# Kernel optimization log

Hardware: AMD Instinct MI355X
Metric: run time of the kernel (lower is better)

Reference implementation:

```python
import jax, jax.numpy as jnp
import numpy as np

M, K, N, R = 8192, 4096, 4096, 64  # tokens, in_features, out_features, pod_rank


def _unpack_int4(packed):
    """Unpack bytes (stored as int32 in [0,256)) into signed int4 values in [-8,7].
    Low nibble is element 2k, high nibble is element 2k+1."""
    b = packed.astype(jnp.int32)
    low = ((b & 0xF) ^ 8) - 8
    high = (((b >> 4) & 0xF) ^ 8) - 8
    out = jnp.stack([low, high], axis=-1)
    return out.reshape(packed.shape[:-1] + (packed.shape[-1] * 2,))


def setup_inputs() -> dict:
    key = jax.random.key(0)
    ks = jax.random.split(key, 7)
    x_quant = jax.random.randint(ks[0], (M, K // 2), 0, 256, dtype=jnp.int32)
    x_scale = jax.random.uniform(ks[1], (M,), dtype=jnp.float32) * 0.01 + 1e-4
    weight = jax.random.randint(ks[2], (N, K // 2), 0, 256, dtype=jnp.int32)
    weight_scales = jax.random.uniform(ks[3], (N, 1), dtype=jnp.float32) * 0.01 + 1e-4
    bias = jax.random.normal(ks[4], (N,), dtype=jnp.float32) * 0.02
    x_r = jax.random.normal(ks[5], (M, R), dtype=jnp.float32)
    w_outlier = jax.random.normal(ks[6], (N, R), dtype=jnp.float32) * 0.02
    return {"x_quant": x_quant, "x_scale": x_scale, "weight": weight,
            "weight_scales": weight_scales, "bias": bias, "x_r": x_r,
            "w_outlier": w_outlier}


def reference(x_quant, x_scale, weight, weight_scales, bias, x_r, w_outlier):
    xi = _unpack_int4(x_quant)          # [M, K] int32 in [-8,7]
    wi = _unpack_int4(weight)           # [N, K] int32 in [-8,7]
    y_int = jnp.matmul(xi, wi.T)        # [M, N] int32 accumulator
    # dequant: per-token activation scale * per-channel weight scale, plus bias
    y = (y_int.astype(jnp.float32) * x_scale[:, None] * weight_scales.reshape(1, -1)
         + bias[None, :])
    # fused low-rank outlier correction: addmm_(x_r, w_outlier.T)
    y = y + jnp.matmul(x_r, w_outlier.T)
    return y
```

## Files before the change

### kernel.cpp

```cpp
#include <hip/hip_runtime.h>
#include <hip/hip_fp16.h>

typedef int      v4i __attribute__((ext_vector_type(4)));
typedef int      v2i __attribute__((ext_vector_type(2)));
typedef float    v4f __attribute__((ext_vector_type(4)));
typedef _Float16 v8h __attribute__((ext_vector_type(8)));
typedef _Float16 v4h __attribute__((ext_vector_type(4)));

#define MDIM 8192
#define NDIM 4096
#define KDIM 4096
#define RDIM 64
#define KW   (KDIM / 2)
#define BM 128
#define BN 128
#define BK 128

typedef const __attribute__((address_space(1))) int* gas_ptr;
typedef __attribute__((address_space(3))) int*       las_ptr;

__device__ __forceinline__ void unpack_w(v4i w, int& lo8, int& hi8) {
    unsigned p01 = __builtin_amdgcn_perm((unsigned)w.y, (unsigned)w.x, 0x0C0C0400u);
    unsigned p23 = __builtin_amdgcn_perm((unsigned)w.w, (unsigned)w.z, 0x0C0C0400u);
    unsigned b4  = __builtin_amdgcn_perm(p23, p01, 0x05040100u);
    unsigned lo = b4 & 0x0F0F0F0Fu;
    unsigned hi = (b4 >> 4) & 0x0F0F0F0Fu;
    lo8 = (int)(((lo ^ 0x08080808u) + 0x78787878u) ^ 0x80808080u);
    hi8 = (int)(((hi ^ 0x08080808u) + 0x78787878u) ^ 0x80808080u);
}

__global__ __launch_bounds__(256)
void repack_int4(const int* __restrict__ xq, const int* __restrict__ wq,
                 char* __restrict__ x8, char* __restrict__ w8)
{
    const size_t XCH = (size_t)MDIM * KW / 4;
    const size_t TCH = XCH + (size_t)NDIM * KW / 4;
    size_t stride = (size_t)gridDim.x * blockDim.x;
    for (size_t i = (size_t)blockIdx.x * blockDim.x + threadIdx.x; i < TCH; i += stride) {
        const int* src;
        char* dst;
        if (i < XCH) { src = xq + i * 4;        dst = x8 + i * 8; }
        else { size_t j = i - XCH; src = wq + j * 4; dst = w8 + j * 8; }
        v4i w = *(const v4i*)src;
        int lo8, hi8;
        unpack_w(w, lo8, hi8);
        *(v2i*)dst = (v2i){lo8, hi8};
    }
}

__global__ __launch_bounds__(256, 3)
void w4a4_gemm(const char* __restrict__ x8, const char* __restrict__ w8,
               const float* __restrict__ xsc, const float* __restrict__ wsc,
               const float* __restrict__ bias, const float* __restrict__ xr,
               const float* __restrict__ wo, float* __restrict__ out)
{
    __shared__ __align__(16) char As[128 * 144];
    __shared__ __align__(16) char Bs[128 * 144];
    __shared__ float xs_s[BM];
    __shared__ float ws_s[BN];
    __shared__ float bs_s[BN];

    const int tid  = threadIdx.x;
    const int lane = tid & 63;
    const int wid  = tid >> 6;
    const int wm   = wid >> 1;
    const int wn   = wid & 1;

    const int swz = (blockIdx.x & 7) * 256 + (blockIdx.x >> 3);
    const int bx  = swz & 31;
    const int by  = swz >> 5;

    if (tid < BM) {
        xs_s[tid] = xsc[by * BM + tid];
    } else {
        int n = tid - BM;
        ws_s[n] = wsc[bx * BN + n];
        bs_s[n] = bias[bx * BN + n];
    }

    const int srow8 = lane >> 3;
    const int scol  = (lane & 7) * 16;
    const char* gA = x8 + (size_t)(by * BM + srow8) * KDIM + scol;
    const char* gB = w8 + (size_t)(bx * BN + srow8) * KDIM + scol;

    v4i acc[4][4];
#pragma unroll
    for (int i = 0; i < 4; ++i)
#pragma unroll
        for (int j = 0; j < 4; ++j) acc[i][j] = (v4i){0, 0, 0, 0};

    const int lr  = lane & 15;
    const int lkb = (lane >> 4) * 16;

    for (int kt = 0; kt < KDIM / BK; ++kt) {
        const size_t kb = (size_t)kt * BK;
#pragma unroll
        for (int q = 0; q < 4; ++q) {
            const int chunk = wid * 4 + q;
            __builtin_amdgcn_global_load_lds(
                (gas_ptr)(const void*)(gA + (size_t)chunk * 8 * KDIM + kb),
                (las_ptr)(void*)(As + chunk * 1024), 16, 0, 0);
            __builtin_amdgcn_global_load_lds(
                (gas_ptr)(const void*)(gB + (size_t)chunk * 8 * KDIM + kb),
                (las_ptr)(void*)(Bs + chunk * 1024), 16, 0, 0);
        }
        __syncthreads();

#pragma unroll
        for (int ks = 0; ks < 2; ++ks) {
            v4i av[4], bv[4];
#pragma unroll
            for (int i = 0; i < 4; ++i)
                av[i] = *(const v4i*)(As + (wm * 64 + i * 16 + lr) * 128 + ks * 64 + lkb);
#pragma unroll
            for (int j = 0; j < 4; ++j)
                bv[j] = *(const v4i*)(Bs + (wn * 64 + j * 16 + lr) * 128 + ks * 64 + lkb);
#pragma unroll
            for (int i = 0; i < 4; ++i)
#pragma unroll
                for (int j = 0; j < 4; ++j)
                    acc[i][j] = __builtin_amdgcn_mfma_i32_16x16x64_i8(av[i], bv[j], acc[i][j], 0, 0, 0);
        }
        __syncthreads();
    }

    v4f facc[4][4];
#pragma unroll
    for (int i = 0; i < 4; ++i) {
        const int row0 = wm * 64 + i * 16 + (lane >> 4) * 4;
#pragma unroll
        for (int j = 0; j < 4; ++j) {
            const int col = wn * 64 + j * 16 + lr;
            const float sw = ws_s[col];
            const float bz = bs_s[col];
#pragma unroll
            for (int r = 0; r < 4; ++r)
                facc[i][j][r] = (float)acc[i][j][r] * xs_s[row0 + r] * sw + bz;
        }
    }

    _Float16* Xh = (_Float16*)As;
    _Float16* Wh = (_Float16*)Bs;
    const int srow   = tid >> 4;
    const int schunk = tid & 15;
#pragma unroll
    for (int p = 0; p < 8; ++p) {
        const int row = p * 16 + srow;
        float4 vx = *(const float4*)(xr + (size_t)(by * BM + row) * RDIM + schunk * 4);
        *(v4h*)(Xh + row * 72 + schunk * 4) =
            (v4h){(_Float16)vx.x, (_Float16)vx.y, (_Float16)vx.z, (_Float16)vx.w};
        float4 vw = *(const float4*)(wo + (size_t)(bx * BN + row) * RDIM + schunk * 4);
        *(v4h*)(Wh + row * 72 + schunk * 4) =
            (v4h){(_Float16)vw.x, (_Float16)vw.y, (_Float16)vw.z, (_Float16)vw.w};
    }
    __syncthreads();

    const int lkh = (lane >> 4) * 8;
#pragma unroll
    for (int ks = 0; ks < 2; ++ks) {
        v8h ah[4], bh[4];
#pragma unroll
        for (int i = 0; i < 4; ++i)
            ah[i] = *(const v8h*)(Xh + (wm * 64 + i * 16 + lr) * 72 + ks * 32 + lkh);
#pragma unroll
        for (int j = 0; j < 4; ++j)
            bh[j] = *(const v8h*)(Wh + (wn * 64 + j * 16 + lr) * 72 + ks * 32 + lkh);
#pragma unroll
        for (int i = 0; i < 4; ++i)
#pragma unroll
            for (int j = 0; j < 4; ++j)
                facc[i][j] = __builtin_amdgcn_mfma_f32_16x16x32_f16(ah[i], bh[j], facc[i][j], 0, 0, 0);
    }

#pragma unroll
    for (int i = 0; i < 4; ++i) {
        const int row0 = wm * 64 + i * 16 + (lane >> 4) * 4;
#pragma unroll
        for (int j = 0; j < 4; ++j) {
            const int col = wn * 64 + j * 16 + lr;
#pragma unroll
            for (int r = 0; r < 4; ++r)
                out[(size_t)(by * BM + row0 + r) * NDIM + (bx * BN + col)] = facc[i][j][r];
        }
    }
}

__global__ __launch_bounds__(256, 2)
void w4a4_fused(const int* __restrict__ xq, const float* __restrict__ xsc,
                const int* __restrict__ wq, const float* __restrict__ wsc,
                const float* __restrict__ bias, const float* __restrict__ xr,
                const float* __restrict__ wo, float* __restrict__ out)
{
    __shared__ __align__(16) char As[BM * 144];
    __shared__ __align__(16) char Bs[BN * 144];
    __shared__ float xs_s[BM];
    __shared__ float ws_s[BN];
    __shared__ float bs_s[BN];

    const int tid  = threadIdx.x;
    const int lane = tid & 63;
    const int wid  = tid >> 6;
    const int wm   = wid >> 1;
    const int wn   = wid & 1;
    const int bx   = blockIdx.x % (NDIM / BN);
    const int by   = blockIdx.x / (NDIM / BN);

    const int srow   = tid >> 4;
    const int schunk = tid & 15;

    if (tid < BM) {
        xs_s[tid] = xsc[by * BM + tid];
    } else {
        int n = tid - 128;
        ws_s[n] = wsc[bx * BN + n];
        bs_s[n] = bias[bx * BN + n];
    }

    const int* gA = xq + (size_t)(by * BM + srow) * KW + schunk * 4;
    const int* gB = wq + (size_t)(bx * BN + srow) * KW + schunk * 4;
    char* lA = As + srow * 144 + schunk * 8;
    char* lB = Bs + srow * 144 + schunk * 8;

    v4i acc[4][4];
#pragma unroll
    for (int i = 0; i < 4; ++i)
#pragma unroll
        for (int j = 0; j < 4; ++j) acc[i][j] = (v4i){0, 0, 0, 0};

    const int lr = lane & 15;
    const int lkb = (lane >> 4) * 16;

    for (int kt = 0; kt < KDIM / BK; ++kt) {
#pragma unroll
        for (int p = 0; p < 8; ++p) {
            v4i w = *(const v4i*)(gA + (size_t)p * 16 * KW + kt * (BK / 2));
            int lo8, hi8;
            unpack_w(w, lo8, hi8);
            *(v2i*)(lA + p * 16 * 144) = (v2i){lo8, hi8};
        }
#pragma unroll
        for (int p = 0; p < 8; ++p) {
            v4i w = *(const v4i*)(gB + (size_t)p * 16 * KW + kt * (BK / 2));
            int lo8, hi8;
            unpack_w(w, lo8, hi8);
            *(v2i*)(lB + p * 16 * 144) = (v2i){lo8, hi8};
        }
        __syncthreads();

#pragma unroll
        for (int ks = 0; ks < 2; ++ks) {
            v4i av[4], bv[4];
#pragma unroll
            for (int i = 0; i < 4; ++i)
                av[i] = *(const v4i*)(As + (wm * 64 + i * 16 + lr) * 144 + ks * 64 + lkb);
#pragma unroll
            for (int j = 0; j < 4; ++j)
                bv[j] = *(const v4i*)(Bs + (wn * 64 + j * 16 + lr) * 144 + ks * 64 + lkb);
#pragma unroll
            for (int i = 0; i < 4; ++i)
#pragma unroll
                for (int j = 0; j < 4; ++j)
                    acc[i][j] = __builtin_amdgcn_mfma_i32_16x16x64_i8(av[i], bv[j], acc[i][j], 0, 0, 0);
        }
        __syncthreads();
    }

    _Float16* Xh = (_Float16*)As;
    _Float16* Wh = (_Float16*)Bs;
#pragma unroll
    for (int p = 0; p < 8; ++p) {
        int row = p * 16 + srow;
        float4 vx = *(const float4*)(xr + (size_t)(by * BM + row) * RDIM + schunk * 4);
        *(v4h*)(Xh + row * 72 + schunk * 4) =
            (v4h){(_Float16)vx.x, (_Float16)vx.y, (_Float16)vx.z, (_Float16)vx.w};
        float4 vw = *(const float4*)(wo + (size_t)(bx * BN + row) * RDIM + schunk * 4);
        *(v4h*)(Wh + row * 72 + schunk * 4) =
            (v4h){(_Float16)vw.x, (_Float16)vw.y, (_Float16)vw.z, (_Float16)vw.w};
    }
    __syncthreads();

    v4f facc[4][4];
#pragma unroll
    for (int i = 0; i < 4; ++i)
#pragma unroll
        for (int j = 0; j < 4; ++j) facc[i][j] = (v4f){0.f, 0.f, 0.f, 0.f};

    const int lkh = (lane >> 4) * 8;
#pragma unroll
    for (int ks = 0; ks < 2; ++ks) {
        v8h ah[4], bh[4];
#pragma unroll
        for (int i = 0; i < 4; ++i)
            ah[i] = *(const v8h*)(Xh + (wm * 64 + i * 16 + lr) * 72 + ks * 32 + lkh);
#pragma unroll
        for (int j = 0; j < 4; ++j)
            bh[j] = *(const v8h*)(Wh + (wn * 64 + j * 16 + lr) * 72 + ks * 32 + lkh);
#pragma unroll
        for (int i = 0; i < 4; ++i)
#pragma unroll
            for (int j = 0; j < 4; ++j)
                facc[i][j] = __builtin_amdgcn_mfma_f32_16x16x32_f16(ah[i], bh[j], facc[i][j], 0, 0, 0);
    }

#pragma unroll
    for (int i = 0; i < 4; ++i) {
        int row0 = wm * 64 + i * 16 + (lane >> 4) * 4;
#pragma unroll
        for (int j = 0; j < 4; ++j) {
            int col = wn * 64 + j * 16 + lr;
            float sw = ws_s[col];
            float bz = bs_s[col];
#pragma unroll
            for (int r = 0; r < 4; ++r) {
                int row = row0 + r;
                float v = (float)acc[i][j][r] * xs_s[row] * sw + bz + facc[i][j][r];
                out[(size_t)(by * BM + row) * NDIM + (bx * BN + col)] = v;
            }
        }
    }
}

extern "C" void kernel_launch(void* const* d_in, const int* in_sizes, int n_in,
                              void* d_out, int out_size, void* d_ws, size_t ws_size,
                              hipStream_t stream) {
    const int*   xq   = (const int*)d_in[0];
    const float* xsc  = (const float*)d_in[1];
    const int*   wq   = (const int*)d_in[2];
    const float* wsc  = (const float*)d_in[3];
    const float* bias = (const float*)d_in[4];
    const float* xr   = (const float*)d_in[5];
    const float* wo   = (const float*)d_in[6];
    float* out = (float*)d_out;

    const size_t X8 = (size_t)MDIM * KDIM;
    const size_t W8 = (size_t)NDIM * KDIM;

    if (ws_size >= X8 + W8) {
        char* x8 = (char*)d_ws;
        char* w8 = x8 + X8;
        repack_int4<<<2048, 256, 0, stream>>>(xq, wq, x8, w8);
        w4a4_gemm<<<(MDIM / BM) * (NDIM / BN), 256, 0, stream>>>(
            x8, w8, xsc, wsc, bias, xr, wo, out);
    } else {
        w4a4_fused<<<(MDIM / BM) * (NDIM / BN), 256, 0, stream>>>(
            xq, xsc, wq, wsc, bias, xr, wo, out);
    }
}
```

Measured before the change: 207.3 us.

## Rewrite int8 GEMM as 256x256 tile, 8-wave, multi-stage pipelined kernel with swizzled LDS

Replaces the 128x128, 4-wave GEMM with a 256x256 tile computed by 512 threads. Global-to-LDS loads are split into 64-byte K sub-stages across a double-buffered ring, and prefetches are issued inside each MFMA phase with explicit vmcnt waits, barriers and setprio. The LDS layout uses an XOR swizzle to avoid bank conflicts, and the fp32 epilogue reuses the accumulator registers to save register pressure. The aim is to hide load latency behind MFMA and cut per-tile global traffic, at the cost of more LDS use, larger register demand and fewer blocks in flight.

```diff
diff --git a/kernel.cpp b/kernel.cpp
--- a/kernel.cpp
+++ b/kernel.cpp
@@ -12,12 +12,10 @@
 #define KDIM 4096
 #define RDIM 64
 #define KW   (KDIM / 2)
-#define BM 128
-#define BN 128
-#define BK 128
-
-typedef const __attribute__((address_space(1))) int* gas_ptr;
-typedef __attribute__((address_space(3))) int*       las_ptr;
+#define NT   (KDIM / 128)
+
+typedef const __attribute__((address_space(1))) char* gas_ptr;
+typedef __attribute__((address_space(3))) char*       las_ptr;
 
 __device__ __forceinline__ void unpack_w(v4i w, int& lo8, int& hi8) {
     unsigned p01 = __builtin_amdgcn_perm((unsigned)w.y, (unsigned)w.x, 0x0C0C0400u);
@@ -39,7 +37,7 @@
     for (size_t i = (size_t)blockIdx.x * blockDim.x + threadIdx.x; i < TCH; i += stride) {
         const int* src;
         char* dst;
-        if (i < XCH) { src = xq + i * 4;        dst = x8 + i * 8; }
+        if (i < XCH) { src = xq + i * 4; dst = x8 + i * 8; }
         else { size_t j = i - XCH; src = wq + j * 4; dst = w8 + j * 8; }
         v4i w = *(const v4i*)src;
         int lo8, hi8;
@@ -48,141 +46,185 @@
     }
 }
 
-__global__ __launch_bounds__(256, 3)
-void w4a4_gemm(const char* __restrict__ x8, const char* __restrict__ w8,
-               const float* __restrict__ xsc, const float* __restrict__ wsc,
-               const float* __restrict__ bias, const float* __restrict__ xr,
-               const float* __restrict__ wo, float* __restrict__ out)
+__device__ __forceinline__ void stage2(const char* g, char* l, int kt, int ks) {
+    const char* s = g + kt * 128 + ks * 64;
+    __builtin_amdgcn_global_load_lds((gas_ptr)(const void*)s,
+                                     (las_ptr)(void*)l, 16, 0, 0);
+    __builtin_amdgcn_global_load_lds((gas_ptr)(const void*)(s + (size_t)128 * KDIM),
+                                     (las_ptr)(void*)(l + 8192), 16, 0, 0);
+}
+
+#define VM4 asm volatile("s_waitcnt vmcnt(4)" ::: "memory")
+#define NOPW
+
+#define PHASE(PAR, MH, KS, STAGE_STMT, WAIT_STMT) do {                          \
+    const char* Ab = &Asub[PAR][KS][0];                                         \
+    const char* Bb = &Bsub[PAR][KS][0];                                         \
+    v4i a_[4], b_[4];                                                           \
+    _Pragma("unroll")                                                           \
+    for (int ii = 0; ii < 4; ++ii)                                              \
+        a_[ii] = *(const v4i*)(Ab + aoff + ((MH) * 4 + ii) * 1024);             \
+    _Pragma("unroll")                                                           \
+    for (int jj = 0; jj < 4; ++jj)                                              \
+        b_[jj] = *(const v4i*)(Bb + boff + jj * 1024);                          \
+    STAGE_STMT;                                                                 \
+    __builtin_amdgcn_s_barrier();                                               \
+    __builtin_amdgcn_s_setprio(1);                                              \
+    _Pragma("unroll")                                                           \
+    for (int ii = 0; ii < 4; ++ii)                                              \
+        _Pragma("unroll")                                                       \
+        for (int jj = 0; jj < 4; ++jj)                                          \
+            acc[(MH) * 4 + ii][jj] = __builtin_amdgcn_mfma_i32_16x16x64_i8(     \
+                a_[ii], b_[jj], acc[(MH) * 4 + ii][jj], 0, 0, 0);               \
+    __builtin_amdgcn_s_setprio(0);                                              \
+    WAIT_STMT;                                                                  \
+    asm volatile("s_barrier" ::: "memory");                                     \
+} while (0)
+
+__global__ __launch_bounds__(512, 2)
+void w4a4_gemm8(const char* __restrict__ x8, const char* __restrict__ w8,
+                const float* __restrict__ xsc, const float* __restrict__ wsc,
+                const float* __restrict__ bias, const float* __restrict__ xr,
+                const float* __restrict__ wo, float* __restrict__ out)
 {
-    __shared__ __align__(16) char As[128 * 144];
-    __shared__ __align__(16) char Bs[128 * 144];
-    __shared__ float xs_s[BM];
-    __shared__ float ws_s[BN];
-    __shared__ float bs_s[BN];
+    __shared__ __align__(16) char Asub[2][2][16384];
+    __shared__ __align__(16) char Bsub[2][2][16384];
+    __shared__ float xs_s[256];
+    __shared__ float ws_s[256];
+    __shared__ float bs_s[256];
 
     const int tid  = threadIdx.x;
     const int lane = tid & 63;
     const int wid  = tid >> 6;
-    const int wm   = wid >> 1;
-    const int wn   = wid & 1;
-
-    const int swz = (blockIdx.x & 7) * 256 + (blockIdx.x >> 3);
-    const int bx  = swz & 31;
-    const int by  = swz >> 5;
-
-    if (tid < BM) {
-        xs_s[tid] = xsc[by * BM + tid];
+    const int wm   = wid >> 2;
+    const int wn   = wid & 3;
+
+    const int s  = (blockIdx.x & 7) * 64 + (blockIdx.x >> 3);
+    const int by = s >> 4;
+    const int bx = s & 15;
+
+    if (tid < 256) {
+        xs_s[tid] = xsc[by * 256 + tid];
     } else {
-        int n = tid - BM;
-        ws_s[n] = wsc[bx * BN + n];
-        bs_s[n] = bias[bx * BN + n];
-    }
-
-    const int srow8 = lane >> 3;
-    const int scol  = (lane & 7) * 16;
-    const char* gA = x8 + (size_t)(by * BM + srow8) * KDIM + scol;
-    const char* gB = w8 + (size_t)(bx * BN + srow8) * KDIM + scol;
-
-    v4i acc[4][4];
-#pragma unroll
-    for (int i = 0; i < 4; ++i)
+        int n = tid - 256;
+        ws_s[n] = wsc[bx * 256 + n];
+        bs_s[n] = bias[bx * 256 + n];
+    }
+
+    const int srow = wid * 16 + (lane >> 2);
+    const int scol = ((lane & 3) * 16) ^ (((lane >> 3) & 3) << 4);
+    const char* gA = x8 + (size_t)(by * 256 + srow) * KDIM + scol;
+    const char* gB = w8 + (size_t)(bx * 256 + srow) * KDIM + scol;
+    const int ldsW = wid * 1024;
+
+    const int lr   = lane & 15;
+    const int cef  = ((lane >> 4) << 4) ^ (((lr >> 1) & 3) << 4);
+    const int aoff = (wm * 128 + lr) * 64 + cef;
+    const int boff = (wn * 64  + lr) * 64 + cef;
+
+    v4i acc[8][4];
+#pragma unroll
+    for (int i = 0; i < 8; ++i)
 #pragma unroll
         for (int j = 0; j < 4; ++j) acc[i][j] = (v4i){0, 0, 0, 0};
 
-    const int lr  = lane & 15;
-    const int lkb = (lane >> 4) * 16;
-
-    for (int kt = 0; kt < KDIM / BK; ++kt) {
-        const size_t kb = (size_t)kt * BK;
-#pragma unroll
-        for (int q = 0; q < 4; ++q) {
-            const int chunk = wid * 4 + q;
-            __builtin_amdgcn_global_load_lds(
-                (gas_ptr)(const void*)(gA + (size_t)chunk * 8 * KDIM + kb),
-                (las_ptr)(void*)(As + chunk * 1024), 16, 0, 0);
-            __builtin_amdgcn_global_load_lds(
-                (gas_ptr)(const void*)(gB + (size_t)chunk * 8 * KDIM + kb),
-                (las_ptr)(void*)(Bs + chunk * 1024), 16, 0, 0);
-        }
-        __syncthreads();
-
-#pragma unroll
-        for (int ks = 0; ks < 2; ++ks) {
-            v4i av[4], bv[4];
-#pragma unroll
-            for (int i = 0; i < 4; ++i)
-                av[i] = *(const v4i*)(As + (wm * 64 + i * 16 + lr) * 128 + ks * 64 + lkb);
-#pragma unroll
-            for (int j = 0; j < 4; ++j)
-                bv[j] = *(const v4i*)(Bs + (wn * 64 + j * 16 + lr) * 128 + ks * 64 + lkb);
-#pragma unroll
-            for (int i = 0; i < 4; ++i)
-#pragma unroll
-                for (int j = 0; j < 4; ++j)
-                    acc[i][j] = __builtin_amdgcn_mfma_i32_16x16x64_i8(av[i], bv[j], acc[i][j], 0, 0, 0);
-        }
-        __syncthreads();
-    }
-
-    v4f facc[4][4];
-#pragma unroll
-    for (int i = 0; i < 4; ++i) {
-        const int row0 = wm * 64 + i * 16 + (lane >> 4) * 4;
+    stage2(gA, &Asub[0][0][ldsW], 0, 0);
+    stage2(gB, &Bsub[0][0][ldsW], 0, 0);
+    stage2(gA, &Asub[0][1][ldsW], 0, 1);
+    stage2(gB, &Bsub[0][1][ldsW], 0, 1);
+    stage2(gA, &Asub[1][0][ldsW], 1, 0);
+    stage2(gB, &Bsub[1][0][ldsW], 1, 0);
+    asm volatile("s_waitcnt vmcnt(4)" ::: "memory");
+    asm volatile("s_barrier" ::: "memory");
+
+    for (int it = 0; it < NT / 2; ++it) {
+        const int kt1 = 2 * it + 1;
+        const int kt2 = (2 * it + 2 < NT) ? 2 * it + 2 : NT - 1;
+        const int kt3 = (2 * it + 3 < NT) ? 2 * it + 3 : NT - 1;
+        PHASE(0, 0, 0, stage2(gA, &Asub[1][1][ldsW], kt1, 1), NOPW);
+        PHASE(0, 1, 0, stage2(gB, &Bsub[1][1][ldsW], kt1, 1), NOPW);
+        PHASE(0, 0, 1, stage2(gA, &Asub[0][0][ldsW], kt2, 0), NOPW);
+        PHASE(0, 1, 1, stage2(gB, &Bsub[0][0][ldsW], kt2, 0), VM4);
+        PHASE(1, 0, 0, stage2(gA, &Asub[0][1][ldsW], kt2, 1), NOPW);
+        PHASE(1, 1, 0, stage2(gB, &Bsub[0][1][ldsW], kt2, 1), NOPW);
+        PHASE(1, 0, 1, stage2(gA, &Asub[1][0][ldsW], kt3, 0), NOPW);
+        PHASE(1, 1, 1, stage2(gB, &Bsub[1][0][ldsW], kt3, 0), VM4);
+    }
+
+    asm volatile("s_waitcnt vmcnt(0)" ::: "memory");
+    asm volatile("s_barrier" ::: "memory");
+
+    _Float16* Xh = (_Float16*)&Asub[0][0][0];
+    _Float16* Wh = (_Float16*)&Bsub[0][0][0];
+    {
+        const int rr = tid >> 3;
+        const int c8 = (tid & 7) * 8;
+#pragma unroll
+        for (int p = 0; p < 4; ++p) {
+            const int row = p * 64 + rr;
+            v4f x0 = *(const v4f*)(xr + (size_t)(by * 256 + row) * RDIM + c8);
+            v4f x1 = *(const v4f*)(xr + (size_t)(by * 256 + row) * RDIM + c8 + 4);
+            v8h hx = {(_Float16)x0[0], (_Float16)x0[1], (_Float16)x0[2], (_Float16)x0[3],
+                      (_Float16)x1[0], (_Float16)x1[1], (_Float16)x1[2], (_Float16)x1[3]};
+            *(v8h*)((char*)Xh + (size_t)row * 144 + c8 * 2) = hx;
+            v4f w0 = *(const v4f*)(wo + (size_t)(bx * 256 + row) * RDIM + c8);
+            v4f w1 = *(const v4f*)(wo + (size_t)(bx * 256 + row) * RDIM + c8 + 4);
+            v8h hw = {(_Float16)w0[0], (_Float16)w0[1], (_Float16)w0[2], (_Float16)w0[3],
+                      (_Float16)w1[0], (_Float16)w1[1], (_Float16)w1[2], (_Float16)w1[3]};
+            *(v8h*)((char*)Wh + (size_t)row * 144 + c8 * 2) = hw;
+        }
+    }
+
+#pragma unroll
+    for (int i = 0; i < 8; ++i) {
+        const int r0 = wm * 128 + i * 16 + ((lane >> 4) << 2);
+        const v4f xs4 = *(const v4f*)&xs_s[r0];
 #pragma unroll
         for (int j = 0; j < 4; ++j) {
             const int col = wn * 64 + j * 16 + lr;
             const float sw = ws_s[col];
             const float bz = bs_s[col];
+            v4f f;
 #pragma unroll
             for (int r = 0; r < 4; ++r)
-                facc[i][j][r] = (float)acc[i][j][r] * xs_s[row0 + r] * sw + bz;
-        }
-    }
-
-    _Float16* Xh = (_Float16*)As;
-    _Float16* Wh = (_Float16*)Bs;
-    const int srow   = tid >> 4;
-    const int schunk = tid & 15;
-#pragma unroll
-    for (int p = 0; p < 8; ++p) {
-        const int row = p * 16 + srow;
-        float4 vx = *(const float4*)(xr + (size_t)(by * BM + row) * RDIM + schunk * 4);
-        *(v4h*)(Xh + row * 72 + schunk * 4) =
-            (v4h){(_Float16)vx.x, (_Float16)vx.y, (_Float16)vx.z, (_Float16)vx.w};
-        float4 vw = *(const float4*)(wo + (size_t)(bx * BN + row) * RDIM + schunk * 4);
-        *(v4h*)(Wh + row * 72 + schunk * 4) =
-            (v4h){(_Float16)vw.x, (_Float16)vw.y, (_Float16)vw.z, (_Float16)vw.w};
+                f[r] = (float)acc[i][j][r] * xs4[r] * sw + bz;
+            acc[i][j] = __builtin_bit_cast(v4i, f);
+        }
     }
     __syncthreads();
 
-    const int lkh = (lane >> 4) * 8;
 #pragma unroll
     for (int ks = 0; ks < 2; ++ks) {
-        v8h ah[4], bh[4];
-#pragma unroll
-        for (int i = 0; i < 4; ++i)
-            ah[i] = *(const v8h*)(Xh + (wm * 64 + i * 16 + lr) * 72 + ks * 32 + lkh);
+        v8h ah[8], bh[4];
+#pragma unroll
+        for (int i = 0; i < 8; ++i)
+            ah[i] = *(const v8h*)((const char*)Xh +
+                     (size_t)(wm * 128 + i * 16 + lr) * 144 + ks * 64 + ((lane >> 4) << 4));
 #pragma unroll
         for (int j = 0; j < 4; ++j)
-            bh[j] = *(const v8h*)(Wh + (wn * 64 + j * 16 + lr) * 72 + ks * 32 + lkh);
-#pragma unroll
-        for (int i = 0; i < 4; ++i)
-#pragma unroll
-            for (int j = 0; j < 4; ++j)
-                facc[i][j] = __builtin_amdgcn_mfma_f32_16x16x32_f16(ah[i], bh[j], facc[i][j], 0, 0, 0);
-    }
-
-#pragma unroll
-    for (int i = 0; i < 4; ++i) {
-        const int row0 = wm * 64 + i * 16 + (lane >> 4) * 4;
+            bh[j] = *(const v8h*)((const char*)Wh +
+                     (size_t)(wn * 64 + j * 16 + lr) * 144 + ks * 64 + ((lane >> 4) << 4));
+#pragma unroll
+        for (int i = 0; i < 8; ++i)
+#pragma unroll
+            for (int j = 0; j < 4; ++j) {
+                v4f c = __builtin_bit_cast(v4f, acc[i][j]);
+                c = __builtin_amdgcn_mfma_f32_16x16x32_f16(ah[i], bh[j], c, 0, 0, 0);
+                acc[i][j] = __builtin_bit_cast(v4i, c);
+            }
+    }
+
+    const size_t obase = (size_t)(by * 256 + wm * 128 + ((lane >> 4) << 2)) * NDIM
+                       + bx * 256 + wn * 64 + lr;
+#pragma unroll
+    for (int i = 0; i < 8; ++i)
 #pragma unroll
         for (int j = 0; j < 4; ++j) {
-            const int col = wn * 64 + j * 16 + lr;
+            v4f f = __builtin_bit_cast(v4f, acc[i][j]);
 #pragma unroll
             for (int r = 0; r < 4; ++r)
-                out[(size_t)(by * BM + row0 + r) * NDIM + (bx * BN + col)] = facc[i][j][r];
-        }
-    }
+                out[obase + (size_t)(i * 16 + r) * NDIM + j * 16] = f[r];
+        }
 }
 
 __global__ __launch_bounds__(256, 2)
@@ -191,33 +233,33 @@
                 const float* __restrict__ bias, const float* __restrict__ xr,
                 const float* __restrict__ wo, float* __restrict__ out)
 {
-    __shared__ __align__(16) char As[BM * 144];
-    __shared__ __align__(16) char Bs[BN * 144];
-    __shared__ float xs_s[BM];
-    __shared__ float ws_s[BN];
-    __shared__ float bs_s[BN];
+    __shared__ __align__(16) char As[128 * 144];
+    __shared__ __align__(16) char Bs[128 * 144];
+    __shared__ float xs_s[128];
+    __shared__ float ws_s[128];
+    __shared__ float bs_s[128];
 
     const int tid  = threadIdx.x;
     const int lane = tid & 63;
     const int wid  = tid >> 6;
     const int wm   = wid >> 1;
     const int wn   = wid & 1;
-    const int bx   = blockIdx.x % (NDIM / BN);
-    const int by   = blockIdx.x / (NDIM / BN);
+    const int bx   = blockIdx.x % (NDIM / 128);
+    const int by   = blockIdx.x / (NDIM / 128);
 
     const int srow   = tid >> 4;
     const int schunk = tid & 15;
 
-    if (tid < BM) {
-        xs_s[tid] = xsc[by * BM + tid];
+    if (tid < 128) {
+        xs_s[tid] = xsc[by * 128 + tid];
     } else {
         int n = tid - 128;
-        ws_s[n] = wsc[bx * BN + n];
-        bs_s[n] = bias[bx * BN + n];
-    }
-
-    const int* gA = xq + (size_t)(by * BM + srow) * KW + schunk * 4;
-    const int* gB = wq + (size_t)(bx * BN + srow) * KW + schunk * 4;
+        ws_s[n] = wsc[bx * 128 + n];
+        bs_s[n] = bias[bx * 128 + n];
+    }
+
+    const int* gA = xq + (size_t)(by * 128 + srow) * KW + schunk * 4;
+    const int* gB = wq + (size_t)(bx * 128 + srow) * KW + schunk * 4;
     char* lA = As + srow * 144 + schunk * 8;
     char* lB = Bs + srow * 144 + schunk * 8;
 
@@ -230,23 +272,22 @@
     const int lr = lane & 15;
     const int lkb = (lane >> 4) * 16;
 
-    for (int kt = 0; kt < KDIM / BK; ++kt) {
+    for (int kt = 0; kt < KDIM / 128; ++kt) {
 #pragma unroll
         for (int p = 0; p < 8; ++p) {
-            v4i w = *(const v4i*)(gA + (size_t)p * 16 * KW + kt * (BK / 2));
+            v4i w = *(const v4i*)(gA + (size_t)p * 16 * KW + kt * 64);
             int lo8, hi8;
             unpack_w(w, lo8, hi8);
             *(v2i*)(lA + p * 16 * 144) = (v2i){lo8, hi8};
         }
 #pragma unroll
         for (int p = 0; p < 8; ++p) {
-            v4i w = *(const v4i*)(gB + (size_t)p * 16 * KW + kt * (BK / 2));
+            v4i w = *(const v4i*)(gB + (size_t)p * 16 * KW + kt * 64);
             int lo8, hi8;
             unpack_w(w, lo8, hi8);
             *(v2i*)(lB + p * 16 * 144) = (v2i){lo8, hi8};
         }
         __syncthreads();
-
 #pragma unroll
         for (int ks = 0; ks < 2; ++ks) {
             v4i av[4], bv[4];
@@ -270,10 +311,10 @@
 #pragma unroll
     for (int p = 0; p < 8; ++p) {
         int row = p * 16 + srow;
-        float4 vx = *(const float4*)(xr + (size_t)(by * BM + row) * RDIM + schunk * 4);
+        float4 vx = *(const float4*)(xr + (size_t)(by * 128 + row) * RDIM + schunk * 4);
         *(v4h*)(Xh + row * 72 + schunk * 4) =
             (v4h){(_Float16)vx.x, (_Float16)vx.y, (_Float16)vx.z, (_Float16)vx.w};
-        float4 vw = *(const float4*)(wo + (size_t)(bx * BN + row) * RDIM + schunk * 4);
+        float4 vw = *(const float4*)(wo + (size_t)(bx * 128 + row) * RDIM + schunk * 4);
         *(v4h*)(Wh + row * 72 + schunk * 4) =
             (v4h){(_Float16)vw.x, (_Float16)vw.y, (_Float16)vw.z, (_Float16)vw.w};
     }
@@ -314,7 +355,7 @@
             for (int r = 0; r < 4; ++r) {
                 int row = row0 + r;
                 float v = (float)acc[i][j][r] * xs_s[row] * sw + bz + facc[i][j][r];
-                out[(size_t)(by * BM + row) * NDIM + (bx * BN + col)] = v;
+                out[(size_t)(by * 128 + row) * NDIM + (bx * 128 + col)] = v;
             }
         }
     }
@@ -339,10 +380,10 @@
         char* x8 = (char*)d_ws;
         char* w8 = x8 + X8;
         repack_int4<<<2048, 256, 0, stream>>>(xq, wq, x8, w8);
-        w4a4_gemm<<<(MDIM / BM) * (NDIM / BN), 256, 0, stream>>>(
+        w4a4_gemm8<<<(MDIM / 256) * (NDIM / 256), 512, 0, stream>>>(
             x8, w8, xsc, wsc, bias, xr, wo, out);
     } else {
-        w4a4_fused<<<(MDIM / BM) * (NDIM / BN), 256, 0, stream>>>(
+        w4a4_fused<<<(MDIM / 128) * (NDIM / 128), 256, 0, stream>>>(
             xq, xsc, wq, wsc, bias, xr, wo, out);
     }
 }
```

New measurement: 172.6 us. 16.8% less time.
